# Performance work log

Hardware: AMD Instinct MI355X
Metric: run time of the kernel (lower is better)

## Reference

```python
import jax, jax.numpy as jnp
import numpy as np

HIDDEN = 4544
N_HEADS = 71
HEAD_DIM = 64
SEQ = 2048
ROPE_BASE = 10000.0


def _rope_cos_sin(seq_len, dim, base=ROPE_BASE):
    inv_freq = 1.0 / (base ** (jnp.arange(0, dim, 2, dtype=jnp.float32) / dim))
    t = jnp.arange(seq_len, dtype=jnp.float32)
    freqs = jnp.einsum('i,j->ij', t, inv_freq)          # [s, dim/2]
    emb = jnp.concatenate([freqs, freqs], axis=-1)      # [s, dim]
    return jnp.cos(emb), jnp.sin(emb)


def _rotate_half(x):
    x1, x2 = jnp.split(x, 2, axis=-1)
    return jnp.concatenate([-x2, x1], axis=-1)


def _apply_rope(x, cos, sin):
    # x: [..., s, d]; cos/sin: [s, d] broadcast over leading dims
    return x * cos + _rotate_half(x) * sin


def setup_inputs() -> dict:
    key = jax.random.key(0)
    k1, k2, k3 = jax.random.split(key, 3)
    hidden_states = jax.random.normal(k1, (1, 1, SEQ, HIDDEN), dtype=jnp.float32) * 0.02
    qkv_weight = jax.random.normal(k2, ((N_HEADS + 2) * HEAD_DIM, HIDDEN), dtype=jnp.float32) * 0.02
    dense_weight = jax.random.normal(k3, (HIDDEN, HIDDEN), dtype=jnp.float32) * 0.02
    # causal additive mask, same construction as the torch module (triu of -1e5)
    mask = jnp.triu(jnp.full((SEQ, SEQ), -100000.0, dtype=jnp.float32), k=1)[None, None]
    return {
        'hidden_states': hidden_states,
        'qkv_weight': qkv_weight,
        'dense_weight': dense_weight,
        'attention_mask': mask,
    }


def reference(hidden_states, qkv_weight, dense_weight, attention_mask):
    b = hidden_states.shape[0]
    s = hidden_states.shape[2]
    x = hidden_states[:, 0]                                   # [b, s, H]

    # fused QKV projection (no bias): [b, s, (nH+2)*d]
    fused = jnp.einsum('bsh,oh->bso', x, qkv_weight)

    q = fused[..., : N_HEADS * HEAD_DIM]
    q = q.reshape(b, s, N_HEADS, HEAD_DIM).transpose(0, 2, 1, 3)   # [b, nH, s, d]
    k = fused[..., N_HEADS * HEAD_DIM : (N_HEADS + 1) * HEAD_DIM]  # [b, s, d] (single KV head, MQA)
    v = fused[..., (N_HEADS + 1) * HEAD_DIM :]                     # [b, s, d]

    cos, sin = _rope_cos_sin(s, HEAD_DIM)
    q = _apply_rope(q, cos, sin)
    k = _apply_rope(k, cos, sin)

    scale = 1.0 / np.sqrt(HEAD_DIM).astype(np.float32)
    scores = jnp.einsum('bhqd,bkd->bhqk', q, k) * scale            # [b, nH, s, s]
    scores = scores + attention_mask
    attn = jax.nn.softmax(scores, axis=-1)
    out = jnp.einsum('bhqk,bkd->bhqd', attn, v)                    # [b, nH, s, d]

    out = out.transpose(0, 2, 1, 3).reshape(b, s, N_HEADS * HEAD_DIM)  # concat heads
    out = jnp.einsum('bsh,oh->bso', out, dense_weight)             # dense projection
    return out[:, None]                                            # [b, 1, s, H]
```

## Files before the change

kernel.cpp:

```cpp
#include <hip/hip_runtime.h>

#define SEQ     2048
#define HIDDEN  4544
#define NHEAD   71
#define HD      64
#define QKV_OUT 4672
#define QKV_PAD 4864
#define HID_PAD 4608

typedef __bf16    bf16;
typedef _Float16  f16;
typedef __bf16    bf16x8 __attribute__((ext_vector_type(8)));
typedef __bf16    bf16x4 __attribute__((ext_vector_type(4)));
typedef _Float16  f16x4  __attribute__((ext_vector_type(4)));
typedef float     f32x4  __attribute__((ext_vector_type(4)));

__device__ inline void gl2lds16(const void* g, void* ldsbase) {
  __builtin_amdgcn_global_load_lds(
      (const __attribute__((address_space(1))) unsigned int*)g,
      (__attribute__((address_space(3))) unsigned int*)ldsbase,
      16, 0, 0);
}

__global__ void cvt_pad_k(const float* __restrict__ in, bf16* __restrict__ out,
                          int ncols4, int nrows, int n4tot) {
  int i = blockIdx.x * blockDim.x + threadIdx.x;
  if (i >= n4tot) return;
  int row = i / ncols4;
  bf16x4 o;
  if (row < nrows) {
    float4 f = ((const float4*)in)[i];
    o[0] = (bf16)f.x; o[1] = (bf16)f.y; o[2] = (bf16)f.z; o[3] = (bf16)f.w;
  } else {
    o[0] = o[1] = o[2] = o[3] = (bf16)0.f;
  }
  *(bf16x4*)(out + (size_t)i * 4) = o;
}

__device__ inline int ldsaddr(int R, int ks, int grp) {
  return (R >> 4) * 1024 + ks * 512 + (R & 15) * 32 + ((grp * 8) ^ (((R >> 3) & 1) << 4));
}

__device__ inline void stage64s(const bf16* mat, int gr0, int kc, int K,
                                bf16* region, int t, int w) {
  const int row = ((t >> 7) << 4) + ((t >> 2) & 15);
  const int ce  = (((t >> 6) & 1) << 5) + ((((t & 3) << 3)) ^ (((t >> 5) & 1) << 4));
  gl2lds16(mat + (size_t)(gr0 + row) * K + kc + ce, region + w * 512);
}

__global__ __launch_bounds__(512) void gemm8p_k(const bf16* __restrict__ A,
                                                const bf16* __restrict__ B,
                                                float* __restrict__ C,
                                                int K, int Nmat, int ldc) {
  __shared__ bf16 lA[2][256 * 64];
  __shared__ bf16 lB[2][256 * 64];
  const int t = threadIdx.x;
  const int lane = t & 63, w = t >> 6;
  const int qi = lane & 15, grp = lane >> 4;
  const int wm = w >> 2, wn = w & 3;

  const int gx = gridDim.x;
  const int nwg = gx * gridDim.y;
  const int orig = blockIdx.y * gx + blockIdx.x;
  const int swz = (orig & 7) * (nwg >> 3) + (orig >> 3);
  const int m0 = (swz % gx) * 256;
  const int n0 = (swz / gx) * 256;

  const int NK = K >> 6;

  stage64s(A, m0 +   0, 0, K, &lA[0][0],        t, w);
  stage64s(A, m0 +  64, 0, K, &lA[0][64 * 64],  t, w);
  stage64s(A, m0 + 128, 0, K, &lA[0][128 * 64], t, w);
  stage64s(A, m0 + 192, 0, K, &lA[0][192 * 64], t, w);
  stage64s(B, n0 +   0, 0, K, &lB[0][0],        t, w);
  stage64s(B, n0 +  64, 0, K, &lB[0][64 * 64],  t, w);
  stage64s(B, n0 + 128, 0, K, &lB[0][128 * 64], t, w);
  stage64s(B, n0 + 192, 0, K, &lB[0][192 * 64], t, w);
  const int k1 = (NK > 1 ? 1 : 0) << 6;
  stage64s(B, n0 +   0, k1, K, &lB[1][0],        t, w);
  stage64s(B, n0 +  64, k1, K, &lB[1][64 * 64],  t, w);
  stage64s(B, n0 + 128, k1, K, &lB[1][128 * 64], t, w);
  stage64s(B, n0 + 192, k1, K, &lB[1][192 * 64], t, w);
  asm volatile("s_waitcnt vmcnt(4)" ::: "memory");
  __builtin_amdgcn_s_barrier();

  f32x4 acc[8][4] = {};
  bf16x8 a[4][2], b0[2][2], b1[2][2];

  for (int kt = 0; kt < NK; ++kt) {
    const int c = kt & 1;
    const int bA = c ^ 1;
    const int kA = (kt + 1 < NK ? kt + 1 : NK - 1) << 6;
    const int kB = (kt + 2 < NK ? kt + 2 : NK - 1) << 6;

#pragma unroll
    for (int i = 0; i < 4; ++i) {
      const int R = wm * 128 + i * 16 + qi;
      a[i][0] = *(const bf16x8*)&lA[c][ldsaddr(R, 0, grp)];
      a[i][1] = *(const bf16x8*)&lA[c][ldsaddr(R, 1, grp)];
    }
#pragma unroll
    for (int j = 0; j < 2; ++j) {
      const int R = wn * 64 + j * 16 + qi;
      b0[j][0] = *(const bf16x8*)&lB[c][ldsaddr(R, 0, grp)];
      b0[j][1] = *(const bf16x8*)&lB[c][ldsaddr(R, 1, grp)];
    }
    stage64s(A, m0 +  0, kA, K, &lA[bA][0],       t, w);
    stage64s(A, m0 + 64, kA, K, &lA[bA][64 * 64], t, w);
    asm volatile("" ::: "memory");
    __builtin_amdgcn_s_barrier();
    asm volatile("s_waitcnt lgkmcnt(0)" ::: "memory");
    __builtin_amdgcn_s_setprio(1);
#pragma unroll
    for (int i = 0; i < 4; ++i)
#pragma unroll
      for (int j = 0; j < 2; ++j) {
        acc[i][j] = __builtin_amdgcn_mfma_f32_16x16x32_bf16(a[i][0], b0[j][0], acc[i][j], 0, 0, 0);
        acc[i][j] = __builtin_amdgcn_mfma_f32_16x16x32_bf16(a[i][1], b0[j][1], acc[i][j], 0, 0, 0);
      }
    __builtin_amdgcn_s_setprio(0);
    __builtin_amdgcn_s_barrier();

#pragma unroll
    for (int j = 0; j < 2; ++j) {
      const int R = wn * 64 + 32 + j * 16 + qi;
      b1[j][0] = *(const bf16x8*)&lB[c][ldsaddr(R, 0, grp)];
      b1[j][1] = *(const bf16x8*)&lB[c][ldsaddr(R, 1, grp)];
    }
    stage64s(A, m0 + 128, kA, K, &lA[bA][128 * 64], t, w);
    stage64s(A, m0 + 192, kA, K, &lA[bA][192 * 64], t, w);
    asm volatile("" ::: "memory");
    __builtin_amdgcn_s_barrier();
    asm volatile("s_waitcnt lgkmcnt(0)" ::: "memory");
    __builtin_amdgcn_s_setprio(1);
#pragma unroll
    for (int i = 0; i < 4; ++i)
#pragma unroll
      for (int j = 0; j < 2; ++j) {
        acc[i][2 + j] = __builtin_amdgcn_mfma_f32_16x16x32_bf16(a[i][0], b1[j][0], acc[i][2 + j], 0, 0, 0);
        acc[i][2 + j] = __builtin_amdgcn_mfma_f32_16x16x32_bf16(a[i][1], b1[j][1], acc[i][2 + j], 0, 0, 0);
      }
    __builtin_amdgcn_s_setprio(0);
    __builtin_amdgcn_s_barrier();

#pragma unroll
    for (int i = 0; i < 4; ++i) {
      const int R = wm * 128 + 64 + i * 16 + qi;
      a[i][0] = *(const bf16x8*)&lA[c][ldsaddr(R, 0, grp)];
      a[i][1] = *(const bf16x8*)&lA[c][ldsaddr(R, 1, grp)];
    }
    stage64s(B, n0 +  0, kB, K, &lB[c][0],       t, w);
    stage64s(B, n0 + 64, kB, K, &lB[c][64 * 64], t, w);
    asm volatile("" ::: "memory");
    __builtin_amdgcn_s_barrier();
    asm volatile("s_waitcnt lgkmcnt(0)" ::: "memory");
    __builtin_amdgcn_s_setprio(1);
#pragma unroll
    for (int i = 0; i < 4; ++i)
#pragma unroll
      for (int j = 0; j < 2; ++j) {
        acc[4 + i][2 + j] = __builtin_amdgcn_mfma_f32_16x16x32_bf16(a[i][0], b1[j][0], acc[4 + i][2 + j], 0, 0, 0);
        acc[4 + i][2 + j] = __builtin_amdgcn_mfma_f32_16x16x32_bf16(a[i][1], b1[j][1], acc[4 + i][2 + j], 0, 0, 0);
      }
    __builtin_amdgcn_s_setprio(0);
    __builtin_amdgcn_s_barrier();

    stage64s(B, n0 + 128, kB, K, &lB[c][128 * 64], t, w);
    stage64s(B, n0 + 192, kB, K, &lB[c][192 * 64], t, w);
    asm volatile("s_waitcnt vmcnt(4)" ::: "memory");
    __builtin_amdgcn_s_barrier();
    __builtin_amdgcn_s_setprio(1);
#pragma unroll
    for (int i = 0; i < 4; ++i)
#pragma unroll
      for (int j = 0; j < 2; ++j) {
        acc[4 + i][j] = __builtin_amdgcn_mfma_f32_16x16x32_bf16(a[i][0], b0[j][0], acc[4 + i][j], 0, 0, 0);
        acc[4 + i][j] = __builtin_amdgcn_mfma_f32_16x16x32_bf16(a[i][1], b0[j][1], acc[4 + i][j], 0, 0, 0);
      }
    __builtin_amdgcn_s_setprio(0);
    __builtin_amdgcn_s_barrier();
  }

#pragma unroll
  for (int mi = 0; mi < 8; ++mi) {
    const int row = m0 + wm * 128 + (mi >> 2) * 64 + (mi & 3) * 16 + grp * 4;
#pragma unroll
    for (int nj = 0; nj < 4; ++nj) {
      const int col = n0 + wn * 64 + (nj >> 1) * 32 + (nj & 1) * 16 + qi;
      if (col < Nmat) {
#pragma unroll
        for (int r = 0; r < 4; ++r)
          C[(size_t)(row + r) * ldc + col] = acc[mi][nj][r];
      }
    }
  }
}

__global__ __launch_bounds__(256) void rope_q_k(const float* __restrict__ fused,
                                                bf16* __restrict__ Qb,
                                                float* __restrict__ cs_tab,
                                                float* __restrict__ sn_tab) {
  const int s = blockIdx.x, t = threadIdx.x;
  __shared__ float cs[64], sn[64];
  if (t < 64) {
    int i = t & 31;
    double invf = pow(10000.0, -(double)i / 32.0);
    double ang = (double)s * invf;
    float c = (float)cos(ang), n = (float)sin(ang);
    cs[t] = c; sn[t] = n;
    cs_tab[s * 64 + t] = c;
    sn_tab[s * 64 + t] = n;
  }
  __syncthreads();
  const float* row = fused + (size_t)s * QKV_OUT;
  for (int e = t; e < HIDDEN; e += 256) {
    int d = e & 63;
    float x = row[e], xp = row[e ^ 32];
    float rot = (d < 32) ? -xp : xp;
    Qb[(size_t)s * HIDDEN + e] = (bf16)((x * cs[d] + rot * sn[d]) * 0.125f);
  }
}

__global__ __launch_bounds__(64) void kvprep_k(const float* __restrict__ fused,
                                               const float* __restrict__ cs_tab,
                                               const float* __restrict__ sn_tab,
                                               bf16* __restrict__ Kf,
                                               f16* __restrict__ Vf) {
  const int t16 = blockIdx.x, lane = threadIdx.x;
  const int qi = lane & 15, grp = lane >> 4;
  const int s = t16 * 16 + qi;
  const float* krow = fused + (size_t)s * QKV_OUT + NHEAD * 64;
  const float* cs = cs_tab + s * 64;
  const float* sn = sn_tab + s * 64;
#pragma unroll
  for (int half = 0; half < 2; ++half) {
    bf16x8 o;
    const int d0 = half * 32 + grp * 8;
#pragma unroll
    for (int j = 0; j < 8; ++j) {
      int d = d0 + j;
      float x = krow[d], xp = krow[d ^ 32];
      float rot = (d < 32) ? -xp : xp;
      o[j] = (bf16)(x * cs[d] + rot * sn[d]);
    }
    *(bf16x8*)&Kf[(t16 * 2 + half) * 512 + lane * 8] = o;
  }
#pragma unroll
  for (int tt = 0; tt < 4; ++tt) {
    f16x4 o;
#pragma unroll
    for (int j = 0; j < 4; ++j)
      o[j] = (f16)fused[(size_t)(t16 * 16 + grp * 4 + j) * QKV_OUT + (NHEAD + 1) * 64 + tt * 16 + qi];
    *(f16x4*)&Vf[t16 * 1024 + tt * 256 + lane * 4] = o;
  }
}

__global__ __launch_bounds__(64) void attn_k(const bf16* __restrict__ Qb,
                                             const bf16* __restrict__ Kf,
                                             const f16*  __restrict__ Vf,
                                             bf16* __restrict__ Ao) {
  __shared__ float fl[2 * 16 * 68];
  const int h = blockIdx.y;
  const int b32 = gridDim.x - 1 - blockIdx.x;
  const int lane = threadIdx.x;
  const int qi = lane & 15, grp = lane >> 4;
  const int q0 = b32 * 32;
  const int lastT = b32 >> 1;

  bf16x8 qf[2][2];
#pragma unroll
  for (int qq = 0; qq < 2; ++qq) {
    const bf16* qb = Qb + (size_t)(q0 + qq * 16 + qi) * HIDDEN + h * 64 + grp * 8;
    qf[qq][0] = *(const bf16x8*)qb;
    qf[qq][1] = *(const bf16x8*)(qb + 32);
  }

  f32x4 o[2][4] = {};
  float l[2] = {0.f, 0.f};

  for (int kb = 0; kb <= lastT; ++kb) {
    const bf16* kfp = Kf + (size_t)kb * 4096 + lane * 8;
    bf16x8 kf[4][2];
#pragma unroll
    for (int kk = 0; kk < 4; ++kk) {
      kf[kk][0] = *(const bf16x8*)(kfp + kk * 1024);
      kf[kk][1] = *(const bf16x8*)(kfp + kk * 1024 + 512);
    }
    f32x4 s4[2][4];
#pragma unroll
    for (int qq = 0; qq < 2; ++qq)
#pragma unroll
      for (int kk = 0; kk < 4; ++kk) {
        f32x4 z = {};
        s4[qq][kk] = __builtin_amdgcn_mfma_f32_16x16x32_bf16(kf[kk][0], qf[qq][0], z, 0, 0, 0);
        s4[qq][kk] = __builtin_amdgcn_mfma_f32_16x16x32_bf16(kf[kk][1], qf[qq][1], s4[qq][kk], 0, 0, 0);
      }
    const f16* vfp = Vf + (size_t)kb * 4096 + lane * 4;
    f16x4 vf[4][4];
#pragma unroll
    for (int kk = 0; kk < 4; ++kk)
#pragma unroll
      for (int tt = 0; tt < 4; ++tt)
        vf[kk][tt] = *(const f16x4*)(vfp + kk * 1024 + tt * 256);

    if (kb == lastT) {
      const int dq = q0 - kb * 64 + qi;
#pragma unroll
      for (int qq = 0; qq < 2; ++qq)
#pragma unroll
        for (int kk = 0; kk < 4; ++kk)
#pragma unroll
          for (int r = 0; r < 4; ++r)
            if (kk * 16 + grp * 4 + r > dq + qq * 16) s4[qq][kk][r] = -1e30f;
    }
    f16x4 pf[2][4];
#pragma unroll
    for (int qq = 0; qq < 2; ++qq) {
      float ls = 0.f;
#pragma unroll
      for (int kk = 0; kk < 4; ++kk) {
        float p0 = __expf(s4[qq][kk][0]), p1 = __expf(s4[qq][kk][1]);
        float p2 = __expf(s4[qq][kk][2]), p3 = __expf(s4[qq][kk][3]);
        ls += (p0 + p1) + (p2 + p3);
        pf[qq][kk][0] = (f16)p0; pf[qq][kk][1] = (f16)p1;
        pf[qq][kk][2] = (f16)p2; pf[qq][kk][3] = (f16)p3;
      }
      l[qq] += ls;
    }
#pragma unroll
    for (int qq = 0; qq < 2; ++qq)
#pragma unroll
      for (int tt = 0; tt < 4; ++tt)
#pragma unroll
        for (int kk = 0; kk < 4; ++kk)
          o[qq][tt] = __builtin_amdgcn_mfma_f32_16x16x16f16(pf[qq][kk], vf[kk][tt], o[qq][tt], 0, 0, 0);
  }

#pragma unroll
  for (int qq = 0; qq < 2; ++qq) {
    float lq = l[qq];
    lq += __shfl_xor(lq, 16);
    lq += __shfl_xor(lq, 32);
    const float inv = 1.0f / lq;
    const float i0 = __shfl(inv, grp * 4 + 0);
    const float i1 = __shfl(inv, grp * 4 + 1);
    const float i2 = __shfl(inv, grp * 4 + 2);
    const float i3 = __shfl(inv, grp * 4 + 3);
    float* flq = fl + qq * 1088;
#pragma unroll
    for (int tt = 0; tt < 4; ++tt) {
      flq[(grp * 4 + 0) * 68 + tt * 16 + qi] = o[qq][tt][0] * i0;
      flq[(grp * 4 + 1) * 68 + tt * 16 + qi] = o[qq][tt][1] * i1;
      flq[(grp * 4 + 2) * 68 + tt * 16 + qi] = o[qq][tt][2] * i2;
      flq[(grp * 4 + 3) * 68 + tt * 16 + qi] = o[qq][tt][3] * i3;
    }
  }
  __syncthreads();
  const int row = lane >> 2, c0 = (lane & 3) * 16;
#pragma unroll
  for (int qq = 0; qq < 2; ++qq) {
    const float* flq = fl + qq * 1088;
    bf16x8 w0, w1;
#pragma unroll
    for (int j = 0; j < 8; ++j) {
      w0[j] = (bf16)flq[row * 68 + c0 + j];
      w1[j] = (bf16)flq[row * 68 + c0 + 8 + j];
    }
    bf16* ob = Ao + (size_t)(q0 + qq * 16 + row) * HIDDEN + h * 64 + c0;
    *(bf16x8*)ob = w0;
    *(bf16x8*)(ob + 8) = w1;
  }
}

extern "C" void kernel_launch(void* const* d_in, const int* in_sizes, int n_in,
                              void* d_out, int out_size, void* d_ws, size_t ws_size,
                              hipStream_t stream) {
  (void)in_sizes; (void)n_in; (void)out_size; (void)ws_size;
  const float* hs   = (const float*)d_in[0];
  const float* wqkv = (const float*)d_in[1];
  const float* wd   = (const float*)d_in[2];
  float* out = (float*)d_out;

  char* ws = (char*)d_ws;
  size_t off = 0;
  auto alloc = [&](size_t b) -> char* {
    char* p = ws + off;
    off += (b + 255) & ~(size_t)255;
    return p;
  };
  bf16* Xb     = (bf16*)alloc((size_t)SEQ * HIDDEN * 2);
  bf16* Wqb    = (bf16*)alloc((size_t)QKV_PAD * HIDDEN * 2);
  bf16* Wdb    = (bf16*)alloc((size_t)HID_PAD * HIDDEN * 2);
  float* fused = (float*)alloc((size_t)SEQ * QKV_OUT * 4);
  bf16* Qb     = (bf16*)alloc((size_t)SEQ * HIDDEN * 2);
  bf16* Kf     = (bf16*)alloc((size_t)(SEQ / 16) * 1024 * 2);
  f16*  Vf     = (f16*)alloc((size_t)(SEQ / 16) * 1024 * 2);
  float* cs_tab = (float*)alloc((size_t)SEQ * 64 * 4);
  float* sn_tab = (float*)alloc((size_t)SEQ * 64 * 4);
  bf16* Ao     = (bf16*)fused;

  const int NC4 = HIDDEN / 4;
  {
    int n4 = SEQ * NC4;
    cvt_pad_k<<<(n4 + 255) / 256, 256, 0, stream>>>(hs, Xb, NC4, SEQ, n4);
    n4 = QKV_PAD * NC4;
    cvt_pad_k<<<(n4 + 255) / 256, 256, 0, stream>>>(wqkv, Wqb, NC4, QKV_OUT, n4);
    n4 = HID_PAD * NC4;
    cvt_pad_k<<<(n4 + 255) / 256, 256, 0, stream>>>(wd, Wdb, NC4, HIDDEN, n4);
  }
  gemm8p_k<<<dim3(SEQ / 256, QKV_PAD / 256), 512, 0, stream>>>(
      Xb, Wqb, fused, HIDDEN, QKV_OUT, QKV_OUT);
  rope_q_k<<<SEQ, 256, 0, stream>>>(fused, Qb, cs_tab, sn_tab);
  kvprep_k<<<SEQ / 16, 64, 0, stream>>>(fused, cs_tab, sn_tab, Kf, Vf);
  attn_k<<<dim3(SEQ / 32, NHEAD), 64, 0, stream>>>(Qb, Kf, Vf, Ao);
  gemm8p_k<<<dim3(SEQ / 256, HID_PAD / 256), 512, 0, stream>>>(
      Ao, Wdb, out, HIDDEN, HIDDEN, HIDDEN);
}
```

Before: 626.1 us.

## Switch GEMM tiles to 256x192 with triple-buffered A staging

Shrinks the GEMM N-tile from 256 to 192 columns and reduces the QKV padding from 4864 to 4800, so less padded work is computed and the grid has more workgroups (200 and 192 instead of 152 and 144) to fill the CUs. The A operand becomes triple-buffered in LDS with a two-stage-ahead prefetch, and the per-iteration schedule is rewritten around 4x3 MFMA sub-blocks per wave. In exchange, each tile reuses its A data across fewer columns, and the deeper pipeline needs a different vmcnt wait and more LDS.

```diff
diff --git a/kernel.cpp b/kernel.cpp
--- a/kernel.cpp
+++ b/kernel.cpp
@@ -5,7 +5,7 @@
 #define NHEAD   71
 #define HD      64
 #define QKV_OUT 4672
-#define QKV_PAD 4864
+#define QKV_PAD 4800
 #define HID_PAD 4608
 
 typedef __bf16    bf16;
@@ -52,8 +52,8 @@
                                                 const bf16* __restrict__ B,
                                                 float* __restrict__ C,
                                                 int K, int Nmat, int ldc) {
-  __shared__ bf16 lA[2][256 * 64];
-  __shared__ bf16 lB[2][256 * 64];
+  __shared__ bf16 lA[3][256 * 64];
+  __shared__ bf16 lB[2][192 * 64];
   const int t = threadIdx.x;
   const int lane = t & 63, w = t >> 6;
   const int qi = lane & 15, grp = lane >> 4;
@@ -64,49 +64,49 @@
   const int orig = blockIdx.y * gx + blockIdx.x;
   const int swz = (orig & 7) * (nwg >> 3) + (orig >> 3);
   const int m0 = (swz % gx) * 256;
-  const int n0 = (swz / gx) * 256;
+  const int n0 = (swz / gx) * 192;
 
   const int NK = K >> 6;
 
-  stage64s(A, m0 +   0, 0, K, &lA[0][0],        t, w);
-  stage64s(A, m0 +  64, 0, K, &lA[0][64 * 64],  t, w);
-  stage64s(A, m0 + 128, 0, K, &lA[0][128 * 64], t, w);
-  stage64s(A, m0 + 192, 0, K, &lA[0][192 * 64], t, w);
-  stage64s(B, n0 +   0, 0, K, &lB[0][0],        t, w);
-  stage64s(B, n0 +  64, 0, K, &lB[0][64 * 64],  t, w);
-  stage64s(B, n0 + 128, 0, K, &lB[0][128 * 64], t, w);
-  stage64s(B, n0 + 192, 0, K, &lB[0][192 * 64], t, w);
+  stage64s(A, m0 +   0, 0, K, &lA[0][0],     t, w);
+  stage64s(A, m0 +  64, 0, K, &lA[0][4096],  t, w);
+  stage64s(A, m0 + 128, 0, K, &lA[0][8192],  t, w);
+  stage64s(A, m0 + 192, 0, K, &lA[0][12288], t, w);
+  stage64s(B, n0 +   0, 0, K, &lB[0][0],     t, w);
+  stage64s(B, n0 +  64, 0, K, &lB[0][4096],  t, w);
+  stage64s(B, n0 + 128, 0, K, &lB[0][8192],  t, w);
   const int k1 = (NK > 1 ? 1 : 0) << 6;
-  stage64s(B, n0 +   0, k1, K, &lB[1][0],        t, w);
-  stage64s(B, n0 +  64, k1, K, &lB[1][64 * 64],  t, w);
-  stage64s(B, n0 + 128, k1, K, &lB[1][128 * 64], t, w);
-  stage64s(B, n0 + 192, k1, K, &lB[1][192 * 64], t, w);
-  asm volatile("s_waitcnt vmcnt(4)" ::: "memory");
+  stage64s(A, m0 +   0, k1, K, &lA[1][0],     t, w);
+  stage64s(A, m0 +  64, k1, K, &lA[1][4096],  t, w);
+  stage64s(A, m0 + 128, k1, K, &lA[1][8192],  t, w);
+  stage64s(A, m0 + 192, k1, K, &lA[1][12288], t, w);
+  stage64s(B, n0 +   0, k1, K, &lB[1][0],     t, w);
+  stage64s(B, n0 +  64, k1, K, &lB[1][4096],  t, w);
+  stage64s(B, n0 + 128, k1, K, &lB[1][8192],  t, w);
+  asm volatile("s_waitcnt vmcnt(7)" ::: "memory");
   __builtin_amdgcn_s_barrier();
 
-  f32x4 acc[8][4] = {};
-  bf16x8 a[4][2], b0[2][2], b1[2][2];
+  f32x4 acc[8][3] = {};
+  bf16x8 bb[3][2];
+  int c3 = 0, s3 = 2;
 
   for (int kt = 0; kt < NK; ++kt) {
-    const int c = kt & 1;
-    const int bA = c ^ 1;
-    const int kA = (kt + 1 < NK ? kt + 1 : NK - 1) << 6;
-    const int kB = (kt + 2 < NK ? kt + 2 : NK - 1) << 6;
-
-#pragma unroll
-    for (int i = 0; i < 4; ++i) {
-      const int R = wm * 128 + i * 16 + qi;
-      a[i][0] = *(const bf16x8*)&lA[c][ldsaddr(R, 0, grp)];
-      a[i][1] = *(const bf16x8*)&lA[c][ldsaddr(R, 1, grp)];
-    }
-#pragma unroll
-    for (int j = 0; j < 2; ++j) {
-      const int R = wn * 64 + j * 16 + qi;
-      b0[j][0] = *(const bf16x8*)&lB[c][ldsaddr(R, 0, grp)];
-      b0[j][1] = *(const bf16x8*)&lB[c][ldsaddr(R, 1, grp)];
-    }
-    stage64s(A, m0 +  0, kA, K, &lA[bA][0],       t, w);
-    stage64s(A, m0 + 64, kA, K, &lA[bA][64 * 64], t, w);
+    const int c2 = kt & 1;
+    const int kf = (kt + 2 < NK ? kt + 2 : NK - 1) << 6;
+    bf16* curA = &lA[c3][0];
+    bf16* curB = &lB[c2][0];
+    bf16* stgA = &lA[s3][0];
+    bf16* stgB = &lB[c2][0];
+    bf16x8 af[4];
+
+#pragma unroll
+    for (int i = 0; i < 4; ++i)
+      af[i] = *(const bf16x8*)&curA[ldsaddr(wm * 128 + i * 16 + qi, 0, grp)];
+#pragma unroll
+    for (int j = 0; j < 3; ++j)
+      bb[j][0] = *(const bf16x8*)&curB[ldsaddr(wn * 48 + j * 16 + qi, 0, grp)];
+    stage64s(A, m0 +  0, kf, K, stgA,        t, w);
+    stage64s(A, m0 + 64, kf, K, stgA + 4096, t, w);
     asm volatile("" ::: "memory");
     __builtin_amdgcn_s_barrier();
     asm volatile("s_waitcnt lgkmcnt(0)" ::: "memory");
@@ -114,21 +114,19 @@
 #pragma unroll
     for (int i = 0; i < 4; ++i)
 #pragma unroll
-      for (int j = 0; j < 2; ++j) {
-        acc[i][j] = __builtin_amdgcn_mfma_f32_16x16x32_bf16(a[i][0], b0[j][0], acc[i][j], 0, 0, 0);
-        acc[i][j] = __builtin_amdgcn_mfma_f32_16x16x32_bf16(a[i][1], b0[j][1], acc[i][j], 0, 0, 0);
-      }
+      for (int j = 0; j < 3; ++j)
+        acc[i][j] = __builtin_amdgcn_mfma_f32_16x16x32_bf16(af[i], bb[j][0], acc[i][j], 0, 0, 0);
     __builtin_amdgcn_s_setprio(0);
     __builtin_amdgcn_s_barrier();
 
 #pragma unroll
-    for (int j = 0; j < 2; ++j) {
-      const int R = wn * 64 + 32 + j * 16 + qi;
-      b1[j][0] = *(const bf16x8*)&lB[c][ldsaddr(R, 0, grp)];
-      b1[j][1] = *(const bf16x8*)&lB[c][ldsaddr(R, 1, grp)];
-    }
-    stage64s(A, m0 + 128, kA, K, &lA[bA][128 * 64], t, w);
-    stage64s(A, m0 + 192, kA, K, &lA[bA][192 * 64], t, w);
+    for (int i = 0; i < 4; ++i)
+      af[i] = *(const bf16x8*)&curA[ldsaddr(wm * 128 + i * 16 + qi, 1, grp)];
+#pragma unroll
+    for (int j = 0; j < 3; ++j)
+      bb[j][1] = *(const bf16x8*)&curB[ldsaddr(wn * 48 + j * 16 + qi, 1, grp)];
+    stage64s(A, m0 + 128, kf, K, stgA + 8192,  t, w);
+    stage64s(A, m0 + 192, kf, K, stgA + 12288, t, w);
     asm volatile("" ::: "memory");
     __builtin_amdgcn_s_barrier();
     asm volatile("s_waitcnt lgkmcnt(0)" ::: "memory");
@@ -136,21 +134,16 @@
 #pragma unroll
     for (int i = 0; i < 4; ++i)
 #pragma unroll
-      for (int j = 0; j < 2; ++j) {
-        acc[i][2 + j] = __builtin_amdgcn_mfma_f32_16x16x32_bf16(a[i][0], b1[j][0], acc[i][2 + j], 0, 0, 0);
-        acc[i][2 + j] = __builtin_amdgcn_mfma_f32_16x16x32_bf16(a[i][1], b1[j][1], acc[i][2 + j], 0, 0, 0);
-      }
+      for (int j = 0; j < 3; ++j)
+        acc[i][j] = __builtin_amdgcn_mfma_f32_16x16x32_bf16(af[i], bb[j][1], acc[i][j], 0, 0, 0);
     __builtin_amdgcn_s_setprio(0);
     __builtin_amdgcn_s_barrier();
 
 #pragma unroll
-    for (int i = 0; i < 4; ++i) {
-      const int R = wm * 128 + 64 + i * 16 + qi;
-      a[i][0] = *(const bf16x8*)&lA[c][ldsaddr(R, 0, grp)];
-      a[i][1] = *(const bf16x8*)&lA[c][ldsaddr(R, 1, grp)];
-    }
-    stage64s(B, n0 +  0, kB, K, &lB[c][0],       t, w);
-    stage64s(B, n0 + 64, kB, K, &lB[c][64 * 64], t, w);
+    for (int i = 0; i < 4; ++i)
+      af[i] = *(const bf16x8*)&curA[ldsaddr(wm * 128 + 64 + i * 16 + qi, 0, grp)];
+    stage64s(B, n0 +  0, kf, K, stgB,        t, w);
+    stage64s(B, n0 + 64, kf, K, stgB + 4096, t, w);
     asm volatile("" ::: "memory");
     __builtin_amdgcn_s_barrier();
     asm volatile("s_waitcnt lgkmcnt(0)" ::: "memory");
@@ -158,39 +151,41 @@
 #pragma unroll
     for (int i = 0; i < 4; ++i)
 #pragma unroll
-      for (int j = 0; j < 2; ++j) {
-        acc[4 + i][2 + j] = __builtin_amdgcn_mfma_f32_16x16x32_bf16(a[i][0], b1[j][0], acc[4 + i][2 + j], 0, 0, 0);
-        acc[4 + i][2 + j] = __builtin_amdgcn_mfma_f32_16x16x32_bf16(a[i][1], b1[j][1], acc[4 + i][2 + j], 0, 0, 0);
-      }
+      for (int j = 0; j < 3; ++j)
+        acc[4 + i][j] = __builtin_amdgcn_mfma_f32_16x16x32_bf16(af[i], bb[j][0], acc[4 + i][j], 0, 0, 0);
     __builtin_amdgcn_s_setprio(0);
     __builtin_amdgcn_s_barrier();
 
-    stage64s(B, n0 + 128, kB, K, &lB[c][128 * 64], t, w);
-    stage64s(B, n0 + 192, kB, K, &lB[c][192 * 64], t, w);
-    asm volatile("s_waitcnt vmcnt(4)" ::: "memory");
-    __builtin_amdgcn_s_barrier();
+#pragma unroll
+    for (int i = 0; i < 4; ++i)
+      af[i] = *(const bf16x8*)&curA[ldsaddr(wm * 128 + 64 + i * 16 + qi, 1, grp)];
+    stage64s(B, n0 + 128, kf, K, stgB + 8192, t, w);
+    asm volatile("s_waitcnt vmcnt(7)" ::: "memory");
+    __builtin_amdgcn_s_barrier();
+    asm volatile("s_waitcnt lgkmcnt(0)" ::: "memory");
     __builtin_amdgcn_s_setprio(1);
 #pragma unroll
     for (int i = 0; i < 4; ++i)
 #pragma unroll
-      for (int j = 0; j < 2; ++j) {
-        acc[4 + i][j] = __builtin_amdgcn_mfma_f32_16x16x32_bf16(a[i][0], b0[j][0], acc[4 + i][j], 0, 0, 0);
-        acc[4 + i][j] = __builtin_amdgcn_mfma_f32_16x16x32_bf16(a[i][1], b0[j][1], acc[4 + i][j], 0, 0, 0);
-      }
+      for (int j = 0; j < 3; ++j)
+        acc[4 + i][j] = __builtin_amdgcn_mfma_f32_16x16x32_bf16(af[i], bb[j][1], acc[4 + i][j], 0, 0, 0);
     __builtin_amdgcn_s_setprio(0);
     __builtin_amdgcn_s_barrier();
-  }
-
-#pragma unroll
-  for (int mi = 0; mi < 8; ++mi) {
-    const int row = m0 + wm * 128 + (mi >> 2) * 64 + (mi & 3) * 16 + grp * 4;
-#pragma unroll
-    for (int nj = 0; nj < 4; ++nj) {
-      const int col = n0 + wn * 64 + (nj >> 1) * 32 + (nj & 1) * 16 + qi;
+
+    c3 = (c3 == 2) ? 0 : c3 + 1;
+    s3 = (s3 == 2) ? 0 : s3 + 1;
+  }
+
+#pragma unroll
+  for (int i = 0; i < 8; ++i) {
+    const int row = m0 + wm * 128 + (i >> 2) * 64 + (i & 3) * 16 + grp * 4;
+#pragma unroll
+    for (int j = 0; j < 3; ++j) {
+      const int col = n0 + wn * 48 + j * 16 + qi;
       if (col < Nmat) {
 #pragma unroll
         for (int r = 0; r < 4; ++r)
-          C[(size_t)(row + r) * ldc + col] = acc[mi][nj][r];
+          C[(size_t)(row + r) * ldc + col] = acc[i][j][r];
       }
     }
   }
@@ -408,11 +403,11 @@
     n4 = HID_PAD * NC4;
     cvt_pad_k<<<(n4 + 255) / 256, 256, 0, stream>>>(wd, Wdb, NC4, HIDDEN, n4);
   }
-  gemm8p_k<<<dim3(SEQ / 256, QKV_PAD / 256), 512, 0, stream>>>(
+  gemm8p_k<<<dim3(SEQ / 256, QKV_PAD / 192), 512, 0, stream>>>(
       Xb, Wqb, fused, HIDDEN, QKV_OUT, QKV_OUT);
   rope_q_k<<<SEQ, 256, 0, stream>>>(fused, Qb, cs_tab, sn_tab);
   kvprep_k<<<SEQ / 16, 64, 0, stream>>>(fused, cs_tab, sn_tab, Kf, Vf);
   attn_k<<<dim3(SEQ / 32, NHEAD), 64, 0, stream>>>(Qb, Kf, Vf, Ao);
-  gemm8p_k<<<dim3(SEQ / 256, HID_PAD / 256), 512, 0, stream>>>(
+  gemm8p_k<<<dim3(SEQ / 256, HID_PAD / 192), 512, 0, stream>>>(
       Ao, Wdb, out, HIDDEN, HIDDEN, HIDDEN);
 }
```

Measured after the change: 599.7 us. 4.2% less time.
